# Optimization experiments

Measured on AMD Instinct MI355X. Metric: run time of the kernel, lower is better.

## Reference

```python
import jax, jax.numpy as jnp
import numpy as np

N, DIM, HID, E = 100000, 128, 512, 600000


def setup_inputs() -> dict:
    key = jax.random.key(0)
    k_h, k_src, k_dst, k_w1, k_b1, k_w2, k_b2 = jax.random.split(key, 7)
    h = jax.random.normal(k_h, (N, DIM), dtype=jnp.float32)
    src = jax.random.randint(k_src, (E,), 0, N)
    dst = jax.random.randint(k_dst, (E,), 0, N)
    edge_index = jnp.stack([src, dst], axis=0).astype(jnp.int64)
    # Linear params stored as [in, out] (math-equivalent to torch's [out,in].T)
    s1 = 1.0 / np.sqrt(2 * DIM)
    s2 = 1.0 / np.sqrt(HID)
    W1 = jax.random.uniform(k_w1, (2 * DIM, HID), jnp.float32, -s1, s1)
    b1 = jax.random.uniform(k_b1, (HID,), jnp.float32, -s1, s1)
    W2 = jax.random.uniform(k_w2, (HID, DIM), jnp.float32, -s2, s2)
    b2 = jax.random.uniform(k_b2, (DIM,), jnp.float32, -s2, s2)
    return {"h": h, "edge_index": edge_index, "W1": W1, "b1": b1, "W2": W2, "b2": b2}


def reference(h, edge_index, W1, b1, W2, b2):
    src, dst = edge_index[0], edge_index[1]
    n = h.shape[0]
    # scatter-mean: sum gathered neighbor features per destination node
    agg_sum = jax.ops.segment_sum(h[src], dst, num_segments=n)  # [N, DIM]
    deg = jax.ops.segment_sum(jnp.ones((src.shape[0],), h.dtype), dst, num_segments=n)  # [N]
    mean = agg_sum / jnp.maximum(deg, 1.0)[:, None]
    # isolated nodes (deg==0) fall back to their own features
    agg = jnp.where((deg == 0)[:, None], h, mean)
    x = jnp.concatenate([h, agg], axis=-1)  # [N, 2*DIM]
    hdn = jax.nn.gelu(x @ W1 + b1, approximate=False)  # torch GELU default = exact erf
    return hdn @ W2 + b2
```

## Files before the change

### kernel.cpp

```cpp
#include <hip/hip_runtime.h>
#include <hip/hip_bf16.h>
#include <math.h>

#define N_NODES 100000
#define DIM 128
#define HID 512
#define EDGES 600000
#define SCAN_CHUNK 1024
#define SCAN_NBLK ((N_NODES + SCAN_CHUNK - 1) / SCAN_CHUNK)
#define MROWS_PAD 100096

typedef short bf16x8 __attribute__((ext_vector_type(8)));
typedef float f32x4 __attribute__((ext_vector_type(4)));

__device__ inline unsigned short f32_to_bf16(float f) {
    unsigned int u = __float_as_uint(f);
    u += 0x7fff + ((u >> 16) & 1);
    return (unsigned short)(u >> 16);
}

__device__ inline void gload16(const void* g, void* l) {
    __builtin_amdgcn_global_load_lds(
        (const __attribute__((address_space(1))) unsigned int*)g,
        (__attribute__((address_space(3))) unsigned int*)l,
        16, 0, 0);
}

__global__ __launch_bounds__(256) void mgl_count_kernel(
    const int* __restrict__ ei, int* __restrict__ cnt)
{
    int e = blockIdx.x * 256 + threadIdx.x;
    if (e < EDGES) atomicAdd(&cnt[ei[EDGES + e]], 1);
}

__global__ __launch_bounds__(256) void mgl_scan_block_kernel(
    const int* __restrict__ cnt, int* __restrict__ row_start, int* __restrict__ bsum)
{
    __shared__ int sdata[256];
    int t = threadIdx.x;
    int base = blockIdx.x * SCAN_CHUNK + t * 4;
    int v[4];
    #pragma unroll
    for (int i = 0; i < 4; ++i) {
        int idx = base + i;
        v[i] = (idx < N_NODES) ? cnt[idx] : 0;
    }
    int tsum = v[0] + v[1] + v[2] + v[3];
    sdata[t] = tsum;
    __syncthreads();
    for (int off = 1; off < 256; off <<= 1) {
        int x = (t >= off) ? sdata[t - off] : 0;
        __syncthreads();
        sdata[t] += x;
        __syncthreads();
    }
    int run = (t > 0) ? sdata[t - 1] : 0;
    #pragma unroll
    for (int i = 0; i < 4; ++i) {
        int idx = base + i;
        if (idx < N_NODES) row_start[idx] = run;
        run += v[i];
    }
    if (t == 255) bsum[blockIdx.x] = sdata[255];
}

__global__ __launch_bounds__(128) void mgl_scan_bsum_kernel(int* __restrict__ bsum)
{
    __shared__ int sd[128];
    int t = threadIdx.x;
    int v = (t < SCAN_NBLK) ? bsum[t] : 0;
    sd[t] = v;
    __syncthreads();
    for (int off = 1; off < 128; off <<= 1) {
        int x = (t >= off) ? sd[t - off] : 0;
        __syncthreads();
        sd[t] += x;
        __syncthreads();
    }
    if (t < SCAN_NBLK) bsum[t] = sd[t] - v;
}

__global__ __launch_bounds__(256) void mgl_scan_add_kernel(
    int* __restrict__ row_start, const int* __restrict__ bsum)
{
    int i = blockIdx.x * 256 + threadIdx.x;
    if (i < N_NODES) row_start[i] += bsum[i / SCAN_CHUNK];
    if (i == 0) row_start[N_NODES] = EDGES;
}

__global__ __launch_bounds__(256) void mgl_fill_kernel(
    const int* __restrict__ ei, const int* __restrict__ row_start,
    int* __restrict__ cursor, int* __restrict__ csr)
{
    int e = blockIdx.x * 256 + threadIdx.x;
    if (e >= EDGES) return;
    int s = ei[e];
    int t = ei[EDGES + e];
    int pos = atomicAdd(&cursor[t], 1);
    csr[row_start[t] + pos] = s;
}

__global__ __launch_bounds__(256) void mgl_convert_h_kernel(
    const float* __restrict__ h, unsigned short* __restrict__ X)
{
    int t = blockIdx.x * 256 + threadIdx.x;
    if (t >= N_NODES * (DIM / 4)) return;
    int node = t >> 5;
    int c4 = t & 31;
    float4 v = *(const float4*)(h + (size_t)node * DIM + c4 * 4);
    ushort4 p;
    p.x = f32_to_bf16(v.x); p.y = f32_to_bf16(v.y);
    p.z = f32_to_bf16(v.z); p.w = f32_to_bf16(v.w);
    *(ushort4*)(X + (size_t)node * 256 + c4 * 4) = p;
}

__global__ __launch_bounds__(256) void mgl_gather_mean_kernel(
    const float* __restrict__ h, const int* __restrict__ row_start,
    const int* __restrict__ csr, unsigned short* __restrict__ X)
{
    int v = blockIdx.x * 4 + (threadIdx.x >> 6);
    if (v >= N_NODES) return;
    int lane = threadIdx.x & 63;
    int beg = row_start[v];
    int end = row_start[v + 1];
    float2 acc = make_float2(0.f, 0.f);
    for (int i = beg; i < end; ++i) {
        int s = csr[i];
        float2 x = *(const float2*)(h + (size_t)s * DIM + lane * 2);
        acc.x += x.x;
        acc.y += x.y;
    }
    float2 res;
    if (end > beg) {
        float inv = 1.f / (float)(end - beg);
        res = make_float2(acc.x * inv, acc.y * inv);
    } else {
        res = *(const float2*)(h + (size_t)v * DIM + lane * 2);
    }
    unsigned int pk = (unsigned int)f32_to_bf16(res.x) |
                      ((unsigned int)f32_to_bf16(res.y) << 16);
    *(unsigned int*)(X + (size_t)v * 256 + 128 + lane * 2) = pk;
}

__global__ __launch_bounds__(256) void mgl_transpose_w1_kernel(
    const float* __restrict__ W1, unsigned short* __restrict__ W1T)
{
    int n = blockIdx.x;
    int k = threadIdx.x;
    W1T[(size_t)n * 256 + k] = f32_to_bf16(W1[(size_t)k * HID + n]);
}

__global__ __launch_bounds__(256) void mgl_transpose_w2_kernel(
    const float* __restrict__ W2, unsigned short* __restrict__ W2T)
{
    int n = blockIdx.x;
    #pragma unroll
    for (int it = 0; it < 2; ++it) {
        int k = threadIdx.x + it * 256;
        W2T[(size_t)n * 512 + k] = f32_to_bf16(W2[(size_t)k * DIM + n]);
    }
}

template<int KTOT, bool GELU_OUT>
__global__ __launch_bounds__(256) void mgl_gemm_kernel(
    const unsigned short* __restrict__ Wt,
    const unsigned short* __restrict__ Xr,
    const float* __restrict__ bias,
    void* __restrict__ outp)
{
    __shared__ unsigned short ldsW[128 * 64];
    __shared__ unsigned short ldsX[128 * 64];

    int tid = threadIdx.x;
    int w = tid >> 6;
    int l = tid & 63;
    int m0 = blockIdx.x * 128;
    int n0 = blockIdx.y * 128;
    int wm = w >> 1;
    int wn = w & 1;
    int r16 = l & 15;
    int kq = l >> 4;

    f32x4 acc[4][4] = {};

    for (int kt = 0; kt < KTOT / 64; ++kt) {
        #pragma unroll
        for (int i = 0; i < 4; ++i) {
            int loff = i * 4096 + w * 1024 + l * 16;
            int row = loff >> 7;
            int c8 = (loff >> 4) & 7;
            const unsigned short* g = Wt + (size_t)(n0 + row) * KTOT + kt * 64 + c8 * 8;
            gload16(g, (char*)ldsW + i * 4096 + w * 1024);
        }
        #pragma unroll
        for (int i = 0; i < 4; ++i) {
            int loff = i * 4096 + w * 1024 + l * 16;
            int row = loff >> 7;
            int c8 = (loff >> 4) & 7;
            int gm = m0 + row;
            if (gm > N_NODES - 1) gm = N_NODES - 1;
            const unsigned short* g = Xr + (size_t)gm * KTOT + kt * 64 + c8 * 8;
            gload16(g, (char*)ldsX + i * 4096 + w * 1024);
        }
        __syncthreads();

        #pragma unroll
        for (int kk = 0; kk < 2; ++kk) {
            bf16x8 a[4], b[4];
            #pragma unroll
            for (int ni = 0; ni < 4; ++ni)
                a[ni] = *(const bf16x8*)((const char*)ldsW +
                          (wn * 64 + ni * 16 + r16) * 128 + kk * 64 + kq * 16);
            #pragma unroll
            for (int mi = 0; mi < 4; ++mi)
                b[mi] = *(const bf16x8*)((const char*)ldsX +
                          (wm * 64 + mi * 16 + r16) * 128 + kk * 64 + kq * 16);
            #pragma unroll
            for (int mi = 0; mi < 4; ++mi)
                #pragma unroll
                for (int ni = 0; ni < 4; ++ni)
                    acc[mi][ni] = __builtin_amdgcn_mfma_f32_16x16x32_bf16(
                        a[ni], b[mi], acc[mi][ni], 0, 0, 0);
        }
        __syncthreads();
    }

    #pragma unroll
    for (int mi = 0; mi < 4; ++mi) {
        int m = m0 + wm * 64 + mi * 16 + r16;
        if (m >= N_NODES) continue;
        #pragma unroll
        for (int ni = 0; ni < 4; ++ni) {
            int nc = n0 + wn * 64 + ni * 16 + kq * 4;
            float4 bv = *(const float4*)(bias + nc);
            float x0 = acc[mi][ni][0] + bv.x;
            float x1 = acc[mi][ni][1] + bv.y;
            float x2 = acc[mi][ni][2] + bv.z;
            float x3 = acc[mi][ni][3] + bv.w;
            if (GELU_OUT) {
                const float s = 0.70710678118654752f;
                float g0 = 0.5f * x0 * (1.0f + erff(x0 * s));
                float g1 = 0.5f * x1 * (1.0f + erff(x1 * s));
                float g2 = 0.5f * x2 * (1.0f + erff(x2 * s));
                float g3 = 0.5f * x3 * (1.0f + erff(x3 * s));
                ushort4 p;
                p.x = f32_to_bf16(g0); p.y = f32_to_bf16(g1);
                p.z = f32_to_bf16(g2); p.w = f32_to_bf16(g3);
                *(ushort4*)((unsigned short*)outp + (size_t)m * HID + nc) = p;
            } else {
                float4 o = make_float4(x0, x1, x2, x3);
                *(float4*)((float*)outp + (size_t)m * DIM + nc) = o;
            }
        }
    }
}

extern "C" void kernel_launch(void* const* d_in, const int* in_sizes, int n_in,
                              void* d_out, int out_size, void* d_ws, size_t ws_size,
                              hipStream_t stream) {
    const float* h  = (const float*)d_in[0];
    const int*   ei = (const int*)d_in[1];
    const float* W1 = (const float*)d_in[2];
    const float* b1 = (const float*)d_in[3];
    const float* W2 = (const float*)d_in[4];
    const float* b2 = (const float*)d_in[5];
    float* out = (float*)d_out;

    unsigned short* X   = (unsigned short*)d_ws;
    unsigned short* hdn = X + (size_t)MROWS_PAD * 256;
    unsigned short* W1T = hdn + (size_t)MROWS_PAD * 512;
    unsigned short* W2T = W1T + 512 * 256;
    int* cnt = (int*)(W2T + 128 * 512);
    int* row_start = cnt + N_NODES;
    int* bsum = row_start + N_NODES + 1;
    int* csr = bsum + 128;

    mgl_transpose_w1_kernel<<<512, 256, 0, stream>>>(W1, W1T);
    mgl_transpose_w2_kernel<<<128, 256, 0, stream>>>(W2, W2T);
    mgl_convert_h_kernel<<<(N_NODES * 32 + 255) / 256, 256, 0, stream>>>(h, X);

    hipMemsetAsync(cnt, 0, N_NODES * sizeof(int), stream);
    mgl_count_kernel<<<(EDGES + 255) / 256, 256, 0, stream>>>(ei, cnt);
    mgl_scan_block_kernel<<<SCAN_NBLK, 256, 0, stream>>>(cnt, row_start, bsum);
    mgl_scan_bsum_kernel<<<1, 128, 0, stream>>>(bsum);
    mgl_scan_add_kernel<<<(N_NODES + 255) / 256, 256, 0, stream>>>(row_start, bsum);
    hipMemsetAsync(cnt, 0, N_NODES * sizeof(int), stream);
    mgl_fill_kernel<<<(EDGES + 255) / 256, 256, 0, stream>>>(ei, row_start, cnt, csr);
    mgl_gather_mean_kernel<<<(N_NODES + 3) / 4, 256, 0, stream>>>(h, row_start, csr, X);

    int mtiles = MROWS_PAD / 128;
    mgl_gemm_kernel<256, true><<<dim3(mtiles, 4), 256, 0, stream>>>(W1T, X, b1, hdn);
    mgl_gemm_kernel<512, false><<<dim3(mtiles, 1), 256, 0, stream>>>(W2T, hdn, b2, out);
}
```

Baseline: 274.0 us.

## Double-buffer GEMM LDS, XOR-swizzle operand layouts, gather from bf16 features

The GEMM now double-buffers its LDS tiles, prefetching the next K tile with global_load_lds while MFMAs run on the current one, using explicit vmcnt waits, raw barriers and a raised wave priority around the compute. All bf16 operands (X, W1T, W2T, hidden) are stored with a row-dependent XOR swizzle so LDS reads avoid bank conflicts. The neighbor gather reads the already-converted bf16 copy of h instead of fp32, halving gather traffic. Block indices are remapped for L2 locality in the first GEMM. Summing bf16 inputs adds some rounding error, and the manual waitcnt scheme depends on an exact count of outstanding loads.

Result: faster. 262.5 us (-4.2%).

```diff
diff --git a/kernel.cpp b/kernel.cpp
--- a/kernel.cpp
+++ b/kernel.cpp
@@ -12,6 +12,7 @@
 
 typedef short bf16x8 __attribute__((ext_vector_type(8)));
 typedef float f32x4 __attribute__((ext_vector_type(4)));
+
 
 __device__ inline unsigned short f32_to_bf16(float f) {
     unsigned int u = __float_as_uint(f);
@@ -111,11 +112,12 @@
     ushort4 p;
     p.x = f32_to_bf16(v.x); p.y = f32_to_bf16(v.y);
     p.z = f32_to_bf16(v.z); p.w = f32_to_bf16(v.w);
-    *(ushort4*)(X + (size_t)node * 256 + c4 * 4) = p;
+    int byteoff = (c4 * 8) ^ ((node & 7) << 4);
+    *(ushort4*)((char*)(X + (size_t)node * 256) + byteoff) = p;
 }
 
 __global__ __launch_bounds__(256) void mgl_gather_mean_kernel(
-    const float* __restrict__ h, const int* __restrict__ row_start,
+    const unsigned short* __restrict__ Xb, const int* __restrict__ row_start,
     const int* __restrict__ csr, unsigned short* __restrict__ X)
 {
     int v = blockIdx.x * 4 + (threadIdx.x >> 6);
@@ -123,23 +125,29 @@
     int lane = threadIdx.x & 63;
     int beg = row_start[v];
     int end = row_start[v + 1];
-    float2 acc = make_float2(0.f, 0.f);
-    for (int i = beg; i < end; ++i) {
-        int s = csr[i];
-        float2 x = *(const float2*)(h + (size_t)s * DIM + lane * 2);
-        acc.x += x.x;
-        acc.y += x.y;
-    }
-    float2 res;
+    int laneByte = lane * 4;
+    const char* xb = (const char*)Xb;
+
     if (end > beg) {
+        float2 acc = make_float2(0.f, 0.f);
+        for (int i = beg; i < end; ++i) {
+            int s = csr[i];
+            unsigned int pk = *(const unsigned int*)(
+                xb + (size_t)s * 512 + (laneByte ^ ((s & 7) << 4)));
+            acc.x += __uint_as_float(pk << 16);
+            acc.y += __uint_as_float(pk & 0xffff0000u);
+        }
         float inv = 1.f / (float)(end - beg);
-        res = make_float2(acc.x * inv, acc.y * inv);
+        unsigned int po = (unsigned int)f32_to_bf16(acc.x * inv) |
+                          ((unsigned int)f32_to_bf16(acc.y * inv) << 16);
+        *(unsigned int*)((char*)(X + (size_t)v * 256) +
+                         ((256 + laneByte) ^ ((v & 7) << 4))) = po;
     } else {
-        res = *(const float2*)(h + (size_t)v * DIM + lane * 2);
-    }
-    unsigned int pk = (unsigned int)f32_to_bf16(res.x) |
-                      ((unsigned int)f32_to_bf16(res.y) << 16);
-    *(unsigned int*)(X + (size_t)v * 256 + 128 + lane * 2) = pk;
+        unsigned int pk = *(const unsigned int*)(
+            xb + (size_t)v * 512 + (laneByte ^ ((v & 7) << 4)));
+        *(unsigned int*)((char*)(X + (size_t)v * 256) +
+                         ((256 + laneByte) ^ ((v & 7) << 4))) = pk;
+    }
 }
 
 __global__ __launch_bounds__(256) void mgl_transpose_w1_kernel(
@@ -147,7 +155,9 @@
 {
     int n = blockIdx.x;
     int k = threadIdx.x;
-    W1T[(size_t)n * 256 + k] = f32_to_bf16(W1[(size_t)k * HID + n]);
+    unsigned short val = f32_to_bf16(W1[(size_t)k * HID + n]);
+    int byteoff = (k * 2) ^ ((n & 7) << 4);
+    *(unsigned short*)((char*)(W1T + (size_t)n * 256) + byteoff) = val;
 }
 
 __global__ __launch_bounds__(256) void mgl_transpose_w2_kernel(
@@ -157,64 +167,94 @@
     #pragma unroll
     for (int it = 0; it < 2; ++it) {
         int k = threadIdx.x + it * 256;
-        W2T[(size_t)n * 512 + k] = f32_to_bf16(W2[(size_t)k * DIM + n]);
-    }
-}
-
-template<int KTOT, bool GELU_OUT>
+        unsigned short val = f32_to_bf16(W2[(size_t)k * DIM + n]);
+        int byteoff = (k * 2) ^ ((n & 7) << 4);
+        *(unsigned short*)((char*)(W2T + (size_t)n * 512) + byteoff) = val;
+    }
+}
+
+template<int KTOT, int NY, bool GELU_OUT>
 __global__ __launch_bounds__(256) void mgl_gemm_kernel(
     const unsigned short* __restrict__ Wt,
     const unsigned short* __restrict__ Xr,
     const float* __restrict__ bias,
     void* __restrict__ outp)
 {
-    __shared__ unsigned short ldsW[128 * 64];
-    __shared__ unsigned short ldsX[128 * 64];
+    constexpr int NT = KTOT / 64;
+    __shared__ unsigned short ldsW[2][128 * 64];
+    __shared__ unsigned short ldsX[2][128 * 64];
 
     int tid = threadIdx.x;
     int w = tid >> 6;
     int l = tid & 63;
-    int m0 = blockIdx.x * 128;
-    int n0 = blockIdx.y * 128;
+
+    int bid = blockIdx.x;
+    if (NY > 1) {
+        int cpx = gridDim.x >> 3;
+        bid = (bid & 7) * cpx + (bid >> 3);
+    }
+    int m0 = (bid / NY) * 128;
+    int n0 = (bid % NY) * 128;
+
     int wm = w >> 1;
     int wn = w & 1;
     int r16 = l & 15;
     int kq = l >> 4;
+    int rowmask = (r16 & 7) << 4;
 
     f32x4 acc[4][4] = {};
 
-    for (int kt = 0; kt < KTOT / 64; ++kt) {
+    int loff_row[4], loff_col[4];
+    #pragma unroll
+    for (int i = 0; i < 4; ++i) {
+        int loff = i * 4096 + w * 1024 + l * 16;
+        loff_row[i] = loff >> 7;
+        loff_col[i] = loff & 127;
+    }
+
+    auto STAGE = [&](int buf, int kt) {
         #pragma unroll
         for (int i = 0; i < 4; ++i) {
-            int loff = i * 4096 + w * 1024 + l * 16;
-            int row = loff >> 7;
-            int c8 = (loff >> 4) & 7;
-            const unsigned short* g = Wt + (size_t)(n0 + row) * KTOT + kt * 64 + c8 * 8;
-            gload16(g, (char*)ldsW + i * 4096 + w * 1024);
+            const char* g = (const char*)Wt +
+                (size_t)(n0 + loff_row[i]) * (KTOT * 2) + kt * 128 + loff_col[i];
+            gload16(g, (char*)&ldsW[buf][0] + i * 4096 + w * 1024);
         }
         #pragma unroll
         for (int i = 0; i < 4; ++i) {
-            int loff = i * 4096 + w * 1024 + l * 16;
-            int row = loff >> 7;
-            int c8 = (loff >> 4) & 7;
-            int gm = m0 + row;
+            int gm = m0 + loff_row[i];
             if (gm > N_NODES - 1) gm = N_NODES - 1;
-            const unsigned short* g = Xr + (size_t)gm * KTOT + kt * 64 + c8 * 8;
-            gload16(g, (char*)ldsX + i * 4096 + w * 1024);
-        }
-        __syncthreads();
-
+            const char* g = (const char*)Xr +
+                (size_t)gm * (KTOT * 2) + kt * 128 + loff_col[i];
+            gload16(g, (char*)&ldsX[buf][0] + i * 4096 + w * 1024);
+        }
+    };
+
+    STAGE(0, 0);
+
+    for (int kt = 0; kt < NT; ++kt) {
+        int cur = kt & 1;
+        if (kt + 1 < NT) {
+            STAGE(cur ^ 1, kt + 1);
+            asm volatile("s_waitcnt vmcnt(8)" ::: "memory");
+        } else {
+            asm volatile("s_waitcnt vmcnt(0)" ::: "memory");
+        }
+        __builtin_amdgcn_s_barrier();
+        asm volatile("" ::: "memory");
+
+        const char* bW = (const char*)&ldsW[cur][0];
+        const char* bX = (const char*)&ldsX[cur][0];
+        __builtin_amdgcn_s_setprio(1);
         #pragma unroll
         for (int kk = 0; kk < 2; ++kk) {
+            int posb = (kk * 64 + kq * 16) ^ rowmask;
             bf16x8 a[4], b[4];
             #pragma unroll
             for (int ni = 0; ni < 4; ++ni)
-                a[ni] = *(const bf16x8*)((const char*)ldsW +
-                          (wn * 64 + ni * 16 + r16) * 128 + kk * 64 + kq * 16);
+                a[ni] = *(const bf16x8*)(bW + (wn * 64 + ni * 16 + r16) * 128 + posb);
             #pragma unroll
             for (int mi = 0; mi < 4; ++mi)
-                b[mi] = *(const bf16x8*)((const char*)ldsX +
-                          (wm * 64 + mi * 16 + r16) * 128 + kk * 64 + kq * 16);
+                b[mi] = *(const bf16x8*)(bX + (wm * 64 + mi * 16 + r16) * 128 + posb);
             #pragma unroll
             for (int mi = 0; mi < 4; ++mi)
                 #pragma unroll
@@ -222,7 +262,9 @@
                     acc[mi][ni] = __builtin_amdgcn_mfma_f32_16x16x32_bf16(
                         a[ni], b[mi], acc[mi][ni], 0, 0, 0);
         }
-        __syncthreads();
+        __builtin_amdgcn_s_setprio(0);
+        __builtin_amdgcn_s_barrier();
+        asm volatile("" ::: "memory");
     }
 
     #pragma unroll
@@ -246,7 +288,9 @@
                 ushort4 p;
                 p.x = f32_to_bf16(g0); p.y = f32_to_bf16(g1);
                 p.z = f32_to_bf16(g2); p.w = f32_to_bf16(g3);
-                *(ushort4*)((unsigned short*)outp + (size_t)m * HID + nc) = p;
+                unsigned short* row = (unsigned short*)outp + (size_t)m * HID;
+                int byteoff = (nc * 2) ^ ((m & 7) << 4);
+                *(ushort4*)((char*)row + byteoff) = p;
             } else {
                 float4 o = make_float4(x0, x1, x2, x3);
                 *(float4*)((float*)outp + (size_t)m * DIM + nc) = o;
@@ -286,9 +330,9 @@
     mgl_scan_add_kernel<<<(N_NODES + 255) / 256, 256, 0, stream>>>(row_start, bsum);
     hipMemsetAsync(cnt, 0, N_NODES * sizeof(int), stream);
     mgl_fill_kernel<<<(EDGES + 255) / 256, 256, 0, stream>>>(ei, row_start, cnt, csr);
-    mgl_gather_mean_kernel<<<(N_NODES + 3) / 4, 256, 0, stream>>>(h, row_start, csr, X);
+    mgl_gather_mean_kernel<<<(N_NODES + 3) / 4, 256, 0, stream>>>(X, row_start, csr, X);
 
     int mtiles = MROWS_PAD / 128;
-    mgl_gemm_kernel<256, true><<<dim3(mtiles, 4), 256, 0, stream>>>(W1T, X, b1, hdn);
-    mgl_gemm_kernel<512, false><<<dim3(mtiles, 1), 256, 0, stream>>>(W2T, hdn, b2, out);
-}
+    mgl_gemm_kernel<256, 4, true><<<mtiles * 4, 256, 0, stream>>>(W1T, X, b1, hdn);
+    mgl_gemm_kernel<512, 1, false><<<mtiles, 256, 0, stream>>>(W2T, hdn, b2, out);
+}
```
